# Optimization experiments

Hardware: AMD Instinct MI355X
Metric: run time of the kernel (lower is better)

The kernel has to match this reference:

```python
import jax, jax.numpy as jnp
import numpy as np

BETA = 0.25


def setup_inputs() -> dict:
    key = jax.random.key(0)
    k1, k2 = jax.random.split(key)
    z_e = jax.random.normal(k1, (16, 64, 64, 64), dtype=jnp.float32)  # (B, D, H, W)
    embedding = jax.random.normal(k2, (1024, 64), dtype=jnp.float32)  # (K, D)
    return {"z_e": z_e, "embedding": embedding}


def reference(z_e, embedding):
    B, D, H, W = z_e.shape
    # (B, D, H, W) -> (B, H, W, D) -> (N, D)
    flat = jnp.transpose(z_e, (0, 2, 3, 1)).reshape(-1, D)
    # squared L2 distances to codebook: (N, K)
    dist = (jnp.sum(flat * flat, axis=1, keepdims=True)
            + jnp.sum(embedding * embedding, axis=1)
            - 2.0 * flat @ embedding.T)
    indices = jnp.argmin(dist, axis=1)  # (N,)
    z_q_flat = embedding[indices]  # (N, D) gather
    z_q = jnp.transpose(z_q_flat.reshape(B, H, W, D), (0, 3, 1, 2))  # (B, D, H, W)
    codebook_loss = jnp.mean((jax.lax.stop_gradient(z_q) - z_e) ** 2)
    commit_loss = jnp.mean((z_q - jax.lax.stop_gradient(z_e)) ** 2)
    vq_loss = codebook_loss + BETA * commit_loss
    # straight-through estimator
    z_q_st = z_e + jax.lax.stop_gradient(z_q - z_e)
    return (z_q_st, vq_loss, indices.reshape(B, H, W))
```

## Files before the change

### kernel.cpp

```cpp
#include <hip/hip_runtime.h>
#include <math.h>

typedef short  short8 __attribute__((ext_vector_type(8)));
typedef float  f32x4  __attribute__((ext_vector_type(4)));

#define ZQ_ELEMS 4194304
#define KC       1024
#define EPS_HALF 0.005f
#define PXB      128


__device__ inline unsigned short bf16_rne(float f) {
    union { float fv; unsigned u; } a; a.fv = f;
    unsigned r = a.u + 0x7FFFu + ((a.u >> 16) & 1u);
    return (unsigned short)(r >> 16);
}
__device__ inline float bf16_to_f(unsigned short h) {
    union { unsigned u; float fv; } a; a.u = ((unsigned)h) << 16;
    return a.fv;
}
__device__ inline double dpack(float hi, unsigned lo) {
    return __hiloint2double(__float_as_int(hi), (int)lo);
}
__device__ inline float dhi(double d) { return __int_as_float(__double2hiint(d)); }
__device__ inline unsigned dlo(double d) { return (unsigned)__double2loint(d); }

__global__ __launch_bounds__(256) void vq_prep(const float* __restrict__ emb,
        unsigned short* __restrict__ epack, float* __restrict__ enorm,
        int* __restrict__ risky_cnt, float* __restrict__ out) {
    const int k = blockIdx.x * 256 + threadIdx.x;
    if (k == 0) { *risky_cnt = 0; out[ZQ_ELEMS] = 0.f; }
    const float4* e4 = (const float4*)(emb + k * 64);
    float s = 0.f;
#pragma unroll
    for (int j = 0; j < 16; ++j) {
        float4 v = e4[j];
        float vv[4] = {v.x, v.y, v.z, v.w};
        ushort4 hv, lv;
        unsigned short h[4], l[4];
#pragma unroll
        for (int t = 0; t < 4; ++t) {
            s = fmaf(vv[t], vv[t], s);
            h[t] = bf16_rne(vv[t]);
            l[t] = bf16_rne(vv[t] - bf16_to_f(h[t]));
        }
        hv.x = h[0]; hv.y = h[1]; hv.z = h[2]; hv.w = h[3];
        lv.x = l[0]; lv.y = l[1]; lv.z = l[2]; lv.w = l[3];
        *(ushort4*)(epack + k * 128 + j * 4)      = hv;
        *(ushort4*)(epack + k * 128 + 64 + j * 4) = lv;
    }
    enorm[k] = s;
}

__global__ __launch_bounds__(256, 2) void vq_scan(const float* __restrict__ z_e,
        const unsigned short* __restrict__ epack, const float* __restrict__ enorm,
        double* __restrict__ pbest, float* __restrict__ pb2) {
    const int tid  = threadIdx.x;
    const int lane = tid & 63;
    const int col  = lane & 15;
    const int g    = lane >> 4;
    const int wv   = __builtin_amdgcn_readfirstlane(tid >> 6);
    const int pxblock = blockIdx.x >> 2;
    const int grp     = blockIdx.x & 3;
    const int cbase   = grp * 256 + wv * 64;
    const int pblk    = pxblock * PXB;

    __shared__ __align__(16) unsigned short afrag[PXB * 128];
    __shared__ double mrgB[4][PXB];
    __shared__ float  mrgS[4][PXB];

    {
        const int lp   = tid & 127;
        const int half = tid >> 7;
        const int pg   = pblk + lp;
        const float* zb = z_e + (pg >> 12) * 262144 + (pg & 4095);
        const int sx = (lp & 7) << 3;
#pragma unroll
        for (int s8 = 0; s8 < 4; ++s8) {
            const int d0 = half * 32 + s8 * 8;
            short8 H, L;
#pragma unroll
            for (int j = 0; j < 8; ++j) {
                float v = zb[(d0 + j) * 4096];
                unsigned short h = bf16_rne(v);
                H[j] = (short)h;
                L[j] = (short)bf16_rne(v - bf16_to_f(h));
            }
            const int sw = d0 ^ sx;
            *(short8*)&afrag[lp * 128 + sw]      = H;
            *(short8*)&afrag[lp * 128 + 64 + sw] = L;
        }
    }

    short8 ah[4][2], al[4][2];
    f32x4 enf[4];
    int clo[4][4];
    const int K1 = 1023 - cbase - g * 4;
#pragma unroll
    for (int t = 0; t < 4; ++t) {
        const int code = cbase + t * 16 + col;
        const short8* ph = (const short8*)(epack + code * 128) + g;
        ah[t][0] = ph[0]; ah[t][1] = ph[4];
        al[t][0] = ph[8]; al[t][1] = ph[12];
        const float4 e4 = *(const float4*)(enorm + cbase + t * 16 + g * 4);
        enf[t][0] = -0.5f * e4.x; enf[t][1] = -0.5f * e4.y;
        enf[t][2] = -0.5f * e4.z; enf[t][3] = -0.5f * e4.w;
#pragma unroll
        for (int r = 0; r < 4; ++r) clo[t][r] = K1 - t * 16 - r;
    }
    __syncthreads();

    const f32x4 zero4 = {0.f, 0.f, 0.f, 0.f};
    const int g8 = g * 8;

#pragma unroll 2
    for (int it = 0; it < PXB / 16; ++it) {
        const int lpx = it * 16 + col;
        const int sxp = (lpx & 7) << 3;
        const unsigned short* ap = &afrag[lpx * 128];
        const short8 bh0 = *(const short8*)&ap[(g8        ) ^ sxp];
        const short8 bh1 = *(const short8*)&ap[(32 + g8   ) ^ sxp];
        const short8 bl0 = *(const short8*)&ap[64 + ((g8     ) ^ sxp)];
        const short8 bl1 = *(const short8*)&ap[64 + ((32 + g8) ^ sxp)];

        double B = dpack(-INFINITY, 0u);
        float  S = -INFINITY;
#pragma unroll
        for (int t = 0; t < 4; ++t) {
            f32x4 aA, aB;
            aA = __builtin_amdgcn_mfma_f32_16x16x32_bf16(ah[t][0], bh0, enf[t], 0, 0, 0);
            aB = __builtin_amdgcn_mfma_f32_16x16x32_bf16(ah[t][1], bh1, zero4, 0, 0, 0);
            aA = __builtin_amdgcn_mfma_f32_16x16x32_bf16(al[t][0], bh0, aA, 0, 0, 0);
            aB = __builtin_amdgcn_mfma_f32_16x16x32_bf16(al[t][1], bh1, aB, 0, 0, 0);
            aA = __builtin_amdgcn_mfma_f32_16x16x32_bf16(ah[t][0], bl0, aA, 0, 0, 0);
            aB = __builtin_amdgcn_mfma_f32_16x16x32_bf16(ah[t][1], bl1, aB, 0, 0, 0);
#pragma unroll
            for (int r = 0; r < 4; ++r) {
                const float v = aA[r] + aB[r];
                S = __builtin_amdgcn_fmed3f(dhi(B), S, v);
                B = fmax(B, dpack(v, (unsigned)clo[t][r]));
            }
        }
#pragma unroll
        for (int s = 16; s < 64; s <<= 1) {
            const double ob = __shfl_xor(B, s, 64);
            const float  o2 = __shfl_xor(S, s, 64);
            S = __builtin_amdgcn_fmed3f(dhi(B), dhi(ob), fmaxf(S, o2));
            B = fmax(B, ob);
        }
        if (g == 0) { mrgB[wv][lpx] = B; mrgS[wv][lpx] = S; }
    }

    __syncthreads();
    if (tid < PXB) {
        double B = mrgB[0][tid];
        float  S = mrgS[0][tid];
#pragma unroll
        for (int w = 1; w < 4; ++w) {
            const double ob = mrgB[w][tid];
            const float  o2 = mrgS[w][tid];
            S = __builtin_amdgcn_fmed3f(dhi(B), dhi(ob), fmaxf(S, o2));
            B = fmax(B, ob);
        }
        const int pxg = pblk + tid;
        pbest[grp * 65536 + pxg] = B;
        pb2[grp * 65536 + pxg]   = S;
    }
}

__global__ __launch_bounds__(256) void vq_final(const float* __restrict__ z_e,
        const float* __restrict__ emb, const double* __restrict__ pbest,
        const float* __restrict__ pb2, float* __restrict__ out,
        int* __restrict__ risky_cnt, int* __restrict__ risky) {
    __shared__ float zq[64][65];
    __shared__ int   sidx[64];
    __shared__ float sred[4];
    const int tid  = threadIdx.x;
    const int lane = tid & 63;
    const int w    = __builtin_amdgcn_readfirstlane(tid >> 6);
    const int pblk = blockIdx.x * 64;
    const int batch = pblk >> 12;
    const int hw0   = pblk & 4095;

    if (w == 0) {
        const int px = pblk + lane;
        double B = pbest[px];
        float  S = pb2[px];
#pragma unroll
        for (int gq = 1; gq < 4; ++gq) {
            const double ob = pbest[gq * 65536 + px];
            const float  o2 = pb2[gq * 65536 + px];
            S = __builtin_amdgcn_fmed3f(dhi(B), dhi(ob), fmaxf(S, o2));
            B = fmax(B, ob);
        }
        const int idx = 1023 - (int)dlo(B);
        sidx[lane] = idx;
        out[ZQ_ELEMS + 1 + px] = (float)idx;
        const bool risk = (dhi(B) - S < EPS_HALF);
        const unsigned long long m = __ballot(risk);
        int base = 0;
        if (lane == 0 && m) base = atomicAdd(risky_cnt, __popcll(m));
        base = __shfl(base, 0, 64);
        if (risk) risky[base + __popcll(m & ((1ull << lane) - 1ull))] = px;
    }
    __syncthreads();

#pragma unroll
    for (int i = 0; i < 16; ++i) {
        const int p = w * 16 + i;
        const int k = sidx[p];
        zq[p][lane] = emb[k * 64 + lane];
    }
    __syncthreads();

    const int p4 = (tid & 15) * 4;
    const float* zeb = z_e + batch * 262144 + hw0;
    float* ob = out + batch * 262144 + hw0;
    float ss = 0.f;
#pragma unroll
    for (int it = 0; it < 4; ++it) {
        const int d = (tid >> 4) + it * 16;
        float4 q;
        q.x = zq[p4 + 0][d]; q.y = zq[p4 + 1][d];
        q.z = zq[p4 + 2][d]; q.w = zq[p4 + 3][d];
        const float4 z = *(const float4*)(zeb + d * 4096 + p4);
        *(float4*)(ob + d * 4096 + p4) = q;
        const float e0 = q.x - z.x, e1 = q.y - z.y, e2 = q.z - z.z, e3 = q.w - z.w;
        ss += e0 * e0 + e1 * e1 + e2 * e2 + e3 * e3;
    }
    for (int off = 32; off; off >>= 1) ss += __shfl_down(ss, off, 64);
    if (lane == 0) sred[w] = ss;
    __syncthreads();
    if (tid == 0)
        atomicAdd(out + ZQ_ELEMS,
                  ((sred[0] + sred[1]) + (sred[2] + sred[3])) * (1.25f / (float)ZQ_ELEMS));
}

__global__ __launch_bounds__(256) void vq_fix(const float* __restrict__ z_e,
        const float* __restrict__ emb, float* __restrict__ out,
        const int* __restrict__ cnt, const int* __restrict__ list) {
    const int n = *cnt;
    if ((int)blockIdx.x * 4 >= n) return;
    __shared__ float etile[64][65];
    const int tid  = threadIdx.x;
    const int lane = tid & 63;
    const int wv   = __builtin_amdgcn_readfirstlane(tid >> 6);

    for (int base = blockIdx.x * 4; base < n; base += gridDim.x * 4) {
        const int item = base + wv;
        const bool active = item < n;
        int pix = 0, oldk = 0;
        float f[64];
        if (active) {
            pix = list[item];
            const float* zb = z_e + (pix >> 12) * 262144 + (pix & 4095);
#pragma unroll
            for (int d = 0; d < 64; ++d) f[d] = zb[d * 4096];
            oldk = (int)out[ZQ_ELEMS + 1 + pix];
        }
        double best = INFINITY; int bk = KC;
        double dold = 0.0;
        for (int j = 0; j < 16; ++j) {
            __syncthreads();
#pragma unroll
            for (int i = 0; i < 16; ++i) {
                const int idx = i * 256 + tid;
                etile[idx >> 6][idx & 63] = emb[j * 4096 + idx];
            }
            __syncthreads();
            if (active) {
                const int k = j * 64 + lane;
                double a0 = 0.0, a1 = 0.0;
#pragma unroll
                for (int d = 0; d < 64; d += 2) {
                    const double d0 = (double)f[d]     - (double)etile[lane][d];
                    const double d1 = (double)f[d + 1] - (double)etile[lane][d + 1];
                    a0 = fma(d0, d0, a0);
                    a1 = fma(d1, d1, a1);
                }
                const double acc = a0 + a1;
                if (acc < best || (acc == best && k < bk)) { best = acc; bk = k; }
                if (k == oldk) dold = acc;
            }
        }
        if (active) {
            for (int off = 32; off; off >>= 1) {
                const double ov = __shfl_down(best, off, 64);
                const int    oi = __shfl_down(bk, off, 64);
                if (ov < best || (ov == best && oi < bk)) { best = ov; bk = oi; }
            }
            for (int off = 32; off; off >>= 1) dold += __shfl_down(dold, off, 64);
            bk   = __shfl(bk, 0, 64);
            best = __shfl(best, 0, 64);
            dold = __shfl(dold, 0, 64);
            if (bk != oldk) {
                if (lane == 0) out[ZQ_ELEMS + 1 + pix] = (float)bk;
                out[(pix >> 12) * 262144 + (pix & 4095) + lane * 4096] = emb[bk * 64 + lane];
                if (lane == 0)
                    atomicAdd(out + ZQ_ELEMS,
                              (float)((best - dold) * (1.25 / (double)ZQ_ELEMS)));
            }
        }
    }
}

extern "C" void kernel_launch(void* const* d_in, const int* in_sizes, int n_in,
                              void* d_out, int out_size, void* d_ws, size_t ws_size,
                              hipStream_t stream) {
    const float* z_e = (const float*)d_in[0];
    const float* emb = (const float*)d_in[1];
    float* out = (float*)d_out;
    char* ws = (char*)d_ws;
    unsigned short* epack = (unsigned short*)ws;
    float*  enorm     = (float*)(ws + 262144);
    int*    risky_cnt = (int*)(ws + 266240);
    int*    risky     = (int*)(ws + 270336);
    double* pbest     = (double*)(ws + 524288);
    float*  pb2       = (float*)(ws + 2621440);

    vq_prep<<<4, 256, 0, stream>>>(emb, epack, enorm, risky_cnt, out);
    vq_scan<<<2048, 256, 0, stream>>>(z_e, epack, enorm, pbest, pb2);
    vq_final<<<1024, 256, 0, stream>>>(z_e, emb, pbest, pb2, out, risky_cnt, risky);
    vq_fix<<<512, 256, 0, stream>>>(z_e, emb, out, risky_cnt, risky);
}
```

Baseline: 84.15 us.

## Fully unroll pixel loop, defer shuffle reductions, alias merge buffers onto afrag LDS

Fully unrolls the 8-iteration pixel loop, keeping per-iteration best/second-best in register arrays so the MFMA chains of different pixel groups can interleave. The cross-lane shuffle reductions then run in a separate pass. The merge buffers are aliased onto the A-fragment shared memory, which needs an extra barrier before they are written, and this cuts LDS per block. The launch-bounds minimum-occupancy hint of 2 is dropped, allowing more registers per thread at possible cost in occupancy.

```diff
diff --git a/kernel.cpp b/kernel.cpp
--- a/kernel.cpp
+++ b/kernel.cpp
@@ -52,7 +52,7 @@
     enorm[k] = s;
 }
 
-__global__ __launch_bounds__(256, 2) void vq_scan(const float* __restrict__ z_e,
+__global__ __launch_bounds__(256) void vq_scan(const float* __restrict__ z_e,
         const unsigned short* __restrict__ epack, const float* __restrict__ enorm,
         double* __restrict__ pbest, float* __restrict__ pb2) {
     const int tid  = threadIdx.x;
@@ -65,9 +65,10 @@
     const int cbase   = grp * 256 + wv * 64;
     const int pblk    = pxblock * PXB;
 
-    __shared__ __align__(16) unsigned short afrag[PXB * 128];
-    __shared__ double mrgB[4][PXB];
-    __shared__ float  mrgS[4][PXB];
+    __shared__ __align__(16) char smem[32768];
+    unsigned short* afrag = (unsigned short*)smem;
+    double* mrgB = (double*)smem;
+    float*  mrgS = (float*)(smem + 4096);
 
     {
         const int lp   = tid & 127;
@@ -113,8 +114,13 @@
     const f32x4 zero4 = {0.f, 0.f, 0.f, 0.f};
     const int g8 = g * 8;
 
-#pragma unroll 2
-    for (int it = 0; it < PXB / 16; ++it) {
+    double Brun[8];
+    float  Srun[8];
+#pragma unroll
+    for (int it = 0; it < 8; ++it) { Brun[it] = dpack(-INFINITY, 0u); Srun[it] = -INFINITY; }
+
+#pragma unroll
+    for (int it = 0; it < 8; ++it) {
         const int lpx = it * 16 + col;
         const int sxp = (lpx & 7) << 3;
         const unsigned short* ap = &afrag[lpx * 128];
@@ -123,8 +129,8 @@
         const short8 bl0 = *(const short8*)&ap[64 + ((g8     ) ^ sxp)];
         const short8 bl1 = *(const short8*)&ap[64 + ((32 + g8) ^ sxp)];
 
-        double B = dpack(-INFINITY, 0u);
-        float  S = -INFINITY;
+        double B = Brun[it];
+        float  S = Srun[it];
 #pragma unroll
         for (int t = 0; t < 4; ++t) {
             f32x4 aA, aB;
@@ -141,6 +147,14 @@
                 B = fmax(B, dpack(v, (unsigned)clo[t][r]));
             }
         }
+        Brun[it] = B;
+        Srun[it] = S;
+    }
+
+#pragma unroll
+    for (int it = 0; it < 8; ++it) {
+        double B = Brun[it];
+        float  S = Srun[it];
 #pragma unroll
         for (int s = 16; s < 64; s <<= 1) {
             const double ob = __shfl_xor(B, s, 64);
@@ -148,17 +162,27 @@
             S = __builtin_amdgcn_fmed3f(dhi(B), dhi(ob), fmaxf(S, o2));
             B = fmax(B, ob);
         }
-        if (g == 0) { mrgB[wv][lpx] = B; mrgS[wv][lpx] = S; }
-    }
-
-    __syncthreads();
+        Brun[it] = B;
+        Srun[it] = S;
+    }
+
+    __syncthreads();
+    if (g == 0) {
+#pragma unroll
+        for (int it = 0; it < 8; ++it) {
+            mrgB[wv * PXB + it * 16 + col] = Brun[it];
+            mrgS[wv * PXB + it * 16 + col] = Srun[it];
+        }
+    }
+    __syncthreads();
+
     if (tid < PXB) {
-        double B = mrgB[0][tid];
-        float  S = mrgS[0][tid];
+        double B = mrgB[tid];
+        float  S = mrgS[tid];
 #pragma unroll
         for (int w = 1; w < 4; ++w) {
-            const double ob = mrgB[w][tid];
-            const float  o2 = mrgS[w][tid];
+            const double ob = mrgB[w * PXB + tid];
+            const float  o2 = mrgS[w * PXB + tid];
             S = __builtin_amdgcn_fmed3f(dhi(B), dhi(ob), fmaxf(S, o2));
             B = fmax(B, ob);
         }
```

Result: slower. 90.03 us (+7.0%).
